# Performance work log

Measured on AMD Instinct MI355X. Metric: run time of the kernel, lower is better.

The kernel has to match this reference:

```python
import jax, jax.numpy as jnp
import numpy as np

EMBED_DIM = 1024

def setup_inputs() -> dict:
    key = jax.random.key(0)
    kx, kq, kk, kv = jax.random.split(key, 4)
    scale = 1.0 / np.sqrt(EMBED_DIM)  # Kaiming-uniform-ish init scale
    x = jax.random.normal(kx, (4, 2048, EMBED_DIM), dtype=jnp.float32)
    Wq = jax.random.uniform(kq, (EMBED_DIM, EMBED_DIM), jnp.float32, -scale, scale)
    Wk = jax.random.uniform(kk, (EMBED_DIM, EMBED_DIM), jnp.float32, -scale, scale)
    Wv = jax.random.uniform(kv, (EMBED_DIM, EMBED_DIM), jnp.float32, -scale, scale)
    return {"x": x, "Wq": Wq, "Wk": Wk, "Wv": Wv}

def reference(x, Wq, Wk, Wv):
    # Linear layers: y = x @ W.T (torch nn.Linear convention, no bias)
    q = jnp.einsum('bsd,ed->bse', x, Wq)
    k = jnp.einsum('bsd,ed->bse', x, Wk)
    v = jnp.einsum('bsd,ed->bse', x, Wv)
    d = k.shape[-1]
    scores = jnp.einsum('bqe,bke->bqk', q, k) / jnp.sqrt(jnp.asarray(d, x.dtype))
    attn = jax.nn.softmax(scores, axis=-1)
    return jnp.einsum('bqk,bke->bqe', attn, v)
```

## Files before the change

kernel.cpp:

```cpp
#include <hip/hip_runtime.h>
#include <hip/hip_bf16.h>

typedef unsigned short u16;
typedef __bf16 bf16x8 __attribute__((ext_vector_type(8)));
typedef float f32x4 __attribute__((ext_vector_type(4)));

__device__ __forceinline__ u16 f2bf(float f) {
    unsigned int u = __builtin_bit_cast(unsigned int, f);
    unsigned int r = u + 0x7FFFu + ((u >> 16) & 1u);
    return (u16)(r >> 16);
}

__device__ __forceinline__ float bf2f(unsigned int bits16) {
    return __builtin_bit_cast(float, bits16 << 16);
}

__device__ __forceinline__ void gload_lds16(const u16* g, u16* l) {
    __builtin_amdgcn_global_load_lds(
        (const __attribute__((address_space(1))) void*)(g),
        (__attribute__((address_space(3))) void*)(l), 16, 0, 0);
}

__global__ __launch_bounds__(256) void cvt_all(
    const float* __restrict__ x, const float* __restrict__ Wq,
    const float* __restrict__ Wk, const float* __restrict__ Wv,
    u16* __restrict__ xb, u16* __restrict__ wqkv)
{
    long long b = blockIdx.x;
    const float* src;
    u16* dst;
    long long i8;
    if (b < 4096) {
        src = x; dst = xb; i8 = b * 256 + threadIdx.x;
    } else {
        int wsel = (int)((b - 4096) >> 9);
        src = (wsel == 0) ? Wq : ((wsel == 1) ? Wk : Wv);
        dst = wqkv + (long long)wsel * 1024 * 1024;
        i8 = ((b - 4096) & 511) * 256 + threadIdx.x;
    }
    const float4* p = (const float4*)src + 2 * i8;
    float4 a = p[0], c = p[1];
    uint4 o;
    o.x = (unsigned)f2bf(a.x) | ((unsigned)f2bf(a.y) << 16);
    o.y = (unsigned)f2bf(a.z) | ((unsigned)f2bf(a.w) << 16);
    o.z = (unsigned)f2bf(c.x) | ((unsigned)f2bf(c.y) << 16);
    o.w = (unsigned)f2bf(c.z) | ((unsigned)f2bf(c.w) << 16);
    ((uint4*)dst)[i8] = o;
}

template <int BN, bool OUT_F32, int EPI>
__global__ __launch_bounds__(512, 2) void gemm4p(
    const u16* __restrict__ A, const u16* __restrict__ B, void* __restrict__ Cv,
    int lda, int ldb, int ldc, int K,
    long long sAz, long long sBz, long long sCz, int cw, int ch,
    float* __restrict__ aux)
{
    constexpr int WC = (BN == 256) ? 4 : 2;
    constexpr int ROWS = (BN == 256) ? 128 : 64;
    constexpr int MI = ROWS / 16;
    constexpr int MIh = MI / 2;
    constexpr int BLOADS = BN / 64;
    constexpr int BNK = BN * 64;

    extern __shared__ u16 lds[];
    u16* ldsB = lds + 32768;

    const int flat = blockIdx.x + gridDim.x * blockIdx.y;
    const int xcd = flat & 7, jj = flat >> 3;
    const int nCx = gridDim.x / cw;
    const int bx = (xcd % nCx) * cw + jj % cw;
    const int by = (xcd / nCx) * ch + jj / cw;

    const int z = blockIdx.z;
    A += (long long)z * sAz;
    B += (long long)z * sBz;

    const int tid  = threadIdx.x;
    const int lane = tid & 63;
    const int wave = tid >> 6;
    const int wr = wave / WC, wc = wave % WC;
    const int m0 = by << 8, n0 = bx * BN;
    const int NT = K >> 6;

    const u16* gAp[4];
    const u16* gBp[BLOADS];
#pragma unroll
    for (int i = 0; i < 4; ++i) {
        int s = tid + i * 512, row = ((s >> 7) << 4) | (s & 15), g = (s >> 4) & 7;
        gAp[i] = A + (long long)(m0 + row) * lda + g * 8;
    }
#pragma unroll
    for (int i = 0; i < BLOADS; ++i) {
        int s = tid + i * 512, row = ((s >> 7) << 4) | (s & 15), g = (s >> 4) & 7;
        gBp[i] = B + (long long)(n0 + row) * ldb + g * 8;
    }
    auto stA = [&](int kt, int buf, int i) {
        gload_lds16(gAp[i] + (long long)kt * 64, lds + buf * 16384 + (tid + i * 512) * 8);
    };
    auto stB = [&](int kt, int buf, int i) {
        gload_lds16(gBp[i] + (long long)kt * 64, ldsB + buf * BNK + (tid + i * 512) * 8);
    };

    f32x4 acc[MI][4] = {};

#pragma unroll
    for (int i = 0; i < 4; ++i) stA(0, 0, i);
#pragma unroll
    for (int i = 0; i < BLOADS; ++i) stB(0, 0, i);
#pragma unroll
    for (int i = 0; i < 4; ++i) stA(1, 1, i);
#pragma unroll
    for (int i = 0; i < BLOADS; ++i) stB(1, 1, i);
    if constexpr (BN == 256) asm volatile("s_waitcnt vmcnt(8)" ::: "memory");
    else                     asm volatile("s_waitcnt vmcnt(6)" ::: "memory");
    __builtin_amdgcn_s_barrier();

#pragma unroll 2
    for (int kt = 0; kt < NT; ++kt) {
        const int cur = kt & 1;
        const u16* sAc = lds  + cur * 16384 + lane * 8;
        const u16* sBc = ldsB + cur * BNK   + lane * 8;
        const bool st = (kt + 2 < NT);

        bf16x8 a[MIh][2], b0[2][2], b1[2][2];

#pragma unroll
        for (int mi = 0; mi < MIh; ++mi)
#pragma unroll
            for (int kk = 0; kk < 2; ++kk)
                a[mi][kk] = *(const bf16x8*)(sAc + ((wr * MI + mi) * 8 + kk * 4) * 128);
#pragma unroll
        for (int ni = 0; ni < 2; ++ni)
#pragma unroll
            for (int kk = 0; kk < 2; ++kk)
                b0[ni][kk] = *(const bf16x8*)(sBc + ((wc * 4 + ni) * 8 + kk * 4) * 128);
        __builtin_amdgcn_s_barrier();
        asm volatile("s_waitcnt lgkmcnt(0)" ::: "memory");
        __builtin_amdgcn_s_setprio(1);
#pragma unroll
        for (int kk = 0; kk < 2; ++kk)
#pragma unroll
            for (int mi = 0; mi < MIh; ++mi)
#pragma unroll
                for (int ni = 0; ni < 2; ++ni)
                    acc[mi][ni] = __builtin_amdgcn_mfma_f32_16x16x32_bf16(
                        a[mi][kk], b0[ni][kk], acc[mi][ni], 0, 0, 0);
        __builtin_amdgcn_s_setprio(0);
        __builtin_amdgcn_s_barrier();

        if constexpr (BN == 256) {
            if (st) { stA(kt + 2, cur, 0); stA(kt + 2, cur, 2); }
        }
#pragma unroll
        for (int ni = 0; ni < 2; ++ni)
#pragma unroll
            for (int kk = 0; kk < 2; ++kk)
                b1[ni][kk] = *(const bf16x8*)(sBc + ((wc * 4 + 2 + ni) * 8 + kk * 4) * 128);
        __builtin_amdgcn_s_barrier();
        asm volatile("s_waitcnt lgkmcnt(0)" ::: "memory");
        __builtin_amdgcn_s_setprio(1);
#pragma unroll
        for (int kk = 0; kk < 2; ++kk)
#pragma unroll
            for (int mi = 0; mi < MIh; ++mi)
#pragma unroll
                for (int ni = 0; ni < 2; ++ni)
                    acc[mi][2 + ni] = __builtin_amdgcn_mfma_f32_16x16x32_bf16(
                        a[mi][kk], b1[ni][kk], acc[mi][2 + ni], 0, 0, 0);
        __builtin_amdgcn_s_setprio(0);
        __builtin_amdgcn_s_barrier();

        if (st) {
            if constexpr (BN == 256) { stB(kt + 2, cur, 0); stB(kt + 2, cur, 1); }
            else                     { stB(kt + 2, cur, 0); }
        }
#pragma unroll
        for (int mi = 0; mi < MIh; ++mi)
#pragma unroll
            for (int kk = 0; kk < 2; ++kk)
                a[mi][kk] = *(const bf16x8*)(sAc + ((wr * MI + MIh + mi) * 8 + kk * 4) * 128);
        __builtin_amdgcn_s_barrier();
        asm volatile("s_waitcnt lgkmcnt(0)" ::: "memory");
        __builtin_amdgcn_s_setprio(1);
#pragma unroll
        for (int kk = 0; kk < 2; ++kk)
#pragma unroll
            for (int mi = 0; mi < MIh; ++mi)
#pragma unroll
                for (int ni = 0; ni < 2; ++ni)
                    acc[MIh + mi][ni] = __builtin_amdgcn_mfma_f32_16x16x32_bf16(
                        a[mi][kk], b0[ni][kk], acc[MIh + mi][ni], 0, 0, 0);
        __builtin_amdgcn_s_setprio(0);
        __builtin_amdgcn_s_barrier();

        if (st) {
            if constexpr (BN == 256) {
                stA(kt + 2, cur, 1); stA(kt + 2, cur, 3);
                stB(kt + 2, cur, 2); stB(kt + 2, cur, 3);
            } else {
                stA(kt + 2, cur, 0); stA(kt + 2, cur, 1);
                stA(kt + 2, cur, 2); stA(kt + 2, cur, 3);
                stB(kt + 2, cur, 1);
            }
        }
        __builtin_amdgcn_s_barrier();
        __builtin_amdgcn_s_setprio(1);
#pragma unroll
        for (int kk = 0; kk < 2; ++kk)
#pragma unroll
            for (int mi = 0; mi < MIh; ++mi)
#pragma unroll
                for (int ni = 0; ni < 2; ++ni)
                    acc[MIh + mi][2 + ni] = __builtin_amdgcn_mfma_f32_16x16x32_bf16(
                        a[mi][kk], b1[ni][kk], acc[MIh + mi][2 + ni], 0, 0, 0);
        __builtin_amdgcn_s_setprio(0);
        if (st) {
            if constexpr (BN == 256) asm volatile("s_waitcnt vmcnt(8)" ::: "memory");
            else                     asm volatile("s_waitcnt vmcnt(6)" ::: "memory");
        } else if (kt + 1 < NT) {
            asm volatile("s_waitcnt vmcnt(0)" ::: "memory");
        }
        __builtin_amdgcn_s_barrier();
    }

    const int fl = lane & 15, fg = lane >> 4;
    const int er0 = m0 + wr * ROWS + fg * 4;
    const int ec0 = n0 + wc * 64 + fl;

    if constexpr (EPI == 1) {
        u16* C = (u16*)Cv + (long long)z * sCz;
        float lsum[MI][4];
#pragma unroll
        for (int mi = 0; mi < MI; ++mi)
#pragma unroll
            for (int j = 0; j < 4; ++j) {
                float s = 0.f;
#pragma unroll
                for (int ni = 0; ni < 4; ++ni) {
                    float e = __expf(acc[mi][ni][j] * 0.03125f);
                    u16 h = f2bf(e);
                    C[(long long)(er0 + mi * 16 + j) * ldc + ec0 + ni * 16] = h;
                    s += bf2f(h);
                }
                lsum[mi][j] = s;
            }
#pragma unroll
        for (int mi = 0; mi < MI; ++mi)
#pragma unroll
            for (int j = 0; j < 4; ++j)
#pragma unroll
                for (int off = 1; off < 16; off <<= 1)
                    lsum[mi][j] += __shfl_xor(lsum[mi][j], off, 64);
        float (*rsbuf)[4] = reinterpret_cast<float(*)[4]>(lds);
        if (fl == 0) {
#pragma unroll
            for (int mi = 0; mi < MI; ++mi)
#pragma unroll
                for (int j = 0; j < 4; ++j)
                    rsbuf[wr * ROWS + mi * 16 + fg * 4 + j][wc] = lsum[mi][j];
        }
        __syncthreads();
        if (tid < 256) {
            float s = rsbuf[tid][0] + rsbuf[tid][1] + rsbuf[tid][2] + rsbuf[tid][3];
            aux[((long long)z * 2048 + m0 + tid) * 8 + bx] = s;
        }
    } else if constexpr (EPI == 2) {
        float* C = (float*)Cv + (long long)z * sCz;
        float iv[MI][4];
#pragma unroll
        for (int mi = 0; mi < MI; ++mi)
#pragma unroll
            for (int j = 0; j < 4; ++j) {
                const float* pr = aux + ((long long)z * 2048 + er0 + mi * 16 + j) * 8;
                float s = 0.f;
#pragma unroll
                for (int k = 0; k < 8; ++k) s += pr[k];
                iv[mi][j] = 1.0f / s;
            }
#pragma unroll
        for (int mi = 0; mi < MI; ++mi)
#pragma unroll
            for (int ni = 0; ni < 4; ++ni)
#pragma unroll
                for (int j = 0; j < 4; ++j)
                    C[(long long)(er0 + mi * 16 + j) * ldc + ec0 + ni * 16] =
                        acc[mi][ni][j] * iv[mi][j];
    } else if constexpr (OUT_F32) {
        float* C = (float*)Cv + (long long)z * sCz;
#pragma unroll
        for (int mi = 0; mi < MI; ++mi)
#pragma unroll
            for (int ni = 0; ni < 4; ++ni)
#pragma unroll
                for (int j = 0; j < 4; ++j)
                    C[(long long)(er0 + mi * 16 + j) * ldc + ec0 + ni * 16] = acc[mi][ni][j];
    } else {
        u16* C = (u16*)Cv + (long long)z * sCz;
#pragma unroll
        for (int mi = 0; mi < MI; ++mi)
#pragma unroll
            for (int ni = 0; ni < 4; ++ni)
#pragma unroll
                for (int j = 0; j < 4; ++j)
                    C[(long long)(er0 + mi * 16 + j) * ldc + ec0 + ni * 16] = f2bf(acc[mi][ni][j]);
    }
}

extern "C" void kernel_launch(void* const* d_in, const int* in_sizes, int n_in,
                              void* d_out, int out_size, void* d_ws, size_t ws_size,
                              hipStream_t stream) {
    const float* x  = (const float*)d_in[0];
    const float* Wq = (const float*)d_in[1];
    const float* Wk = (const float*)d_in[2];
    const float* Wv = (const float*)d_in[3];
    float* out = (float*)d_out;

    const int B = 4, S = 2048, D = 1024;
    const long long MS = (long long)B * S;

    u16* Sc  = (u16*)d_ws;
    u16* xb  = Sc;
    u16* wqk = Sc  + (long long)B * S * S;
    u16* wvb = wqk + 2 * D * D;
    u16* qk  = wvb + D * D;
    u16* vT  = qk  + MS * 2 * D;
    float* partial = (float*)(vT + MS * D);
    size_t need = (size_t)2 * ((long long)B * S * S + 3 * D * D + MS * 2 * D + MS * D)
                + (size_t)4 * (MS * 8);
    if (ws_size < need) return;

    hipFuncSetAttribute(reinterpret_cast<const void*>(&gemm4p<256, false, 0>),
                        hipFuncAttributeMaxDynamicSharedMemorySize, 131072);
    hipFuncSetAttribute(reinterpret_cast<const void*>(&gemm4p<256, false, 1>),
                        hipFuncAttributeMaxDynamicSharedMemorySize, 131072);
    hipFuncSetAttribute(reinterpret_cast<const void*>(&gemm4p<128, false, 0>),
                        hipFuncAttributeMaxDynamicSharedMemorySize, 98304);
    hipFuncSetAttribute(reinterpret_cast<const void*>(&gemm4p<128, true, 2>),
                        hipFuncAttributeMaxDynamicSharedMemorySize, 98304);

    cvt_all<<<4096 + 3 * 512, 256, 0, stream>>>(x, Wq, Wk, Wv, xb, wqk);

    gemm4p<256, false, 0><<<dim3(2 * D / 256, (int)(MS / 256), 1), 512, 131072, stream>>>(
        xb, wqk, qk, D, D, 2 * D, D, 0, 0, 0, 8, 4, nullptr);

    gemm4p<128, false, 0><<<dim3((int)(MS / 128), D / 256, 1), 512, 98304, stream>>>(
        wvb, xb, vT, D, D, (int)MS, D, 0, 0, 0, 8, 4, nullptr);

    gemm4p<256, false, 1><<<dim3(S / 256, S / 256, B), 512, 131072, stream>>>(
        qk, qk + D, Sc, 2 * D, 2 * D, S, D,
        (long long)S * 2 * D, (long long)S * 2 * D, (long long)S * S, 2, 4, partial);

    gemm4p<128, true, 2><<<dim3(D / 128, S / 256, B), 512, 98304, stream>>>(
        Sc, vT, out, S, (int)MS, D, S,
        (long long)S * S, (long long)S, (long long)S * D, 4, 2, partial);
}
```

Measured before the change: 180.2 us.

## Merge QK and V projection GEMMs into one launch and use exp2 in softmax epilogue

The QK projection GEMM (256 tiles) and the transposed V projection GEMM (256 tiles) now run as a single kernel launch, with the block index selecting which GEMM body to run. This removes one launch boundary and the tail drain between the two GEMMs, so both can share the GPU at once. The scores epilogue now uses a native exp2 with a prescaled constant and sums the unrounded float exponentials instead of the bf16-rounded values. The cost is that the merged kernel uses 128KB LDS for both halves, and the row sums no longer exactly match the stored bf16 probabilities.

```diff
diff --git a/kernel.cpp b/kernel.cpp
--- a/kernel.cpp
+++ b/kernel.cpp
@@ -9,10 +9,6 @@
     unsigned int u = __builtin_bit_cast(unsigned int, f);
     unsigned int r = u + 0x7FFFu + ((u >> 16) & 1u);
     return (u16)(r >> 16);
-}
-
-__device__ __forceinline__ float bf2f(unsigned int bits16) {
-    return __builtin_bit_cast(float, bits16 << 16);
 }
 
 __device__ __forceinline__ void gload_lds16(const u16* g, u16* l) {
@@ -49,10 +45,12 @@
 }
 
 template <int BN, bool OUT_F32, int EPI>
-__global__ __launch_bounds__(512, 2) void gemm4p(
+__device__ __forceinline__ void gemm_body(
+    u16* lds,
     const u16* __restrict__ A, const u16* __restrict__ B, void* __restrict__ Cv,
     int lda, int ldb, int ldc, int K,
-    long long sAz, long long sBz, long long sCz, int cw, int ch,
+    long long sAz, long long sBz, long long sCz,
+    int z, int flat, int gx, int cw, int ch,
     float* __restrict__ aux)
 {
     constexpr int WC = (BN == 256) ? 4 : 2;
@@ -62,16 +60,13 @@
     constexpr int BLOADS = BN / 64;
     constexpr int BNK = BN * 64;
 
-    extern __shared__ u16 lds[];
     u16* ldsB = lds + 32768;
 
-    const int flat = blockIdx.x + gridDim.x * blockIdx.y;
     const int xcd = flat & 7, jj = flat >> 3;
-    const int nCx = gridDim.x / cw;
+    const int nCx = gx / cw;
     const int bx = (xcd % nCx) * cw + jj % cw;
     const int by = (xcd / nCx) * ch + jj / cw;
 
-    const int z = blockIdx.z;
     A += (long long)z * sAz;
     B += (long long)z * sBz;
 
@@ -237,10 +232,9 @@
                 float s = 0.f;
 #pragma unroll
                 for (int ni = 0; ni < 4; ++ni) {
-                    float e = __expf(acc[mi][ni][j] * 0.03125f);
-                    u16 h = f2bf(e);
-                    C[(long long)(er0 + mi * 16 + j) * ldc + ec0 + ni * 16] = h;
-                    s += bf2f(h);
+                    float e = __builtin_amdgcn_exp2f(acc[mi][ni][j] * 0.04508422f);
+                    C[(long long)(er0 + mi * 16 + j) * ldc + ec0 + ni * 16] = f2bf(e);
+                    s += e;
                 }
                 lsum[mi][j] = s;
             }
@@ -304,6 +298,36 @@
                 for (int j = 0; j < 4; ++j)
                     C[(long long)(er0 + mi * 16 + j) * ldc + ec0 + ni * 16] = f2bf(acc[mi][ni][j]);
     }
+}
+
+__global__ __launch_bounds__(512, 2) void gemm_fused_qkv_vt(
+    const u16* __restrict__ xb, const u16* __restrict__ wqk,
+    const u16* __restrict__ wvb, u16* __restrict__ qk, u16* __restrict__ vT,
+    int D, int MS)
+{
+    extern __shared__ u16 lds[];
+    const int bid = blockIdx.x;
+    if (bid < 256) {
+        gemm_body<256, false, 0>(lds, xb, wqk, qk, D, D, 2 * D, D,
+                                 0, 0, 0, 0, bid, 8, 8, 4, nullptr);
+    } else {
+        gemm_body<128, false, 0>(lds, wvb, xb, vT, D, D, MS, D,
+                                 0, 0, 0, 0, bid - 256, 64, 8, 4, nullptr);
+    }
+}
+
+template <int BN, bool OUT_F32, int EPI>
+__global__ __launch_bounds__(512, 2) void gemm4p(
+    const u16* __restrict__ A, const u16* __restrict__ B, void* __restrict__ Cv,
+    int lda, int ldb, int ldc, int K,
+    long long sAz, long long sBz, long long sCz, int cw, int ch,
+    float* __restrict__ aux)
+{
+    extern __shared__ u16 lds[];
+    const int flat = blockIdx.x + gridDim.x * blockIdx.y;
+    gemm_body<BN, OUT_F32, EPI>(lds, A, B, Cv, lda, ldb, ldc, K,
+                                sAz, sBz, sCz, blockIdx.z, flat,
+                                gridDim.x, cw, ch, aux);
 }
 
 extern "C" void kernel_launch(void* const* d_in, const int* in_sizes, int n_in,
@@ -329,22 +353,17 @@
                 + (size_t)4 * (MS * 8);
     if (ws_size < need) return;
 
-    hipFuncSetAttribute(reinterpret_cast<const void*>(&gemm4p<256, false, 0>),
+    (void)hipFuncSetAttribute(reinterpret_cast<const void*>(&gemm_fused_qkv_vt),
                         hipFuncAttributeMaxDynamicSharedMemorySize, 131072);
-    hipFuncSetAttribute(reinterpret_cast<const void*>(&gemm4p<256, false, 1>),
+    (void)hipFuncSetAttribute(reinterpret_cast<const void*>(&gemm4p<256, false, 1>),
                         hipFuncAttributeMaxDynamicSharedMemorySize, 131072);
-    hipFuncSetAttribute(reinterpret_cast<const void*>(&gemm4p<128, false, 0>),
+    (void)hipFuncSetAttribute(reinterpret_cast<const void*>(&gemm4p<128, true, 2>),
                         hipFuncAttributeMaxDynamicSharedMemorySize, 98304);
-    hipFuncSetAttribute(reinterpret_cast<const void*>(&gemm4p<128, true, 2>),
-                        hipFuncAttributeMaxDynamicSharedMemorySize, 98304);
 
     cvt_all<<<4096 + 3 * 512, 256, 0, stream>>>(x, Wq, Wk, Wv, xb, wqk);
 
-    gemm4p<256, false, 0><<<dim3(2 * D / 256, (int)(MS / 256), 1), 512, 131072, stream>>>(
-        xb, wqk, qk, D, D, 2 * D, D, 0, 0, 0, 8, 4, nullptr);
-
-    gemm4p<128, false, 0><<<dim3((int)(MS / 128), D / 256, 1), 512, 98304, stream>>>(
-        wvb, xb, vT, D, D, (int)MS, D, 0, 0, 0, 8, 4, nullptr);
+    gemm_fused_qkv_vt<<<512, 512, 131072, stream>>>(
+        xb, wqk, wvb, qk, vT, D, (int)MS);
 
     gemm4p<256, false, 1><<<dim3(S / 256, S / 256, B), 512, 131072, stream>>>(
         qk, qk + D, Sc, 2 * D, 2 * D, S, D,
```

New measurement: 176.1 us, median of 2. 2.3% less time.
